# Kernel optimization log

Measured on AMD Instinct MI355X. Metric: run time of the kernel, lower is better.

The kernel has to match this reference:

```python
import jax, jax.numpy as jnp
import numpy as np

N_NODES = 100000
N_EDGES = 1600000
IN_DIM = 64
HID_DIM = 32


def setup_inputs() -> dict:
    key = jax.random.key(0)
    k1, k2, k3, k4 = jax.random.split(key, 4)
    features = jax.random.normal(k1, (N_NODES, IN_DIM), dtype=jnp.float32)
    src = jax.random.randint(k2, (N_EDGES,), 0, N_NODES, dtype=jnp.int32)
    dst = jax.random.randint(k3, (N_EDGES,), 0, N_NODES, dtype=jnp.int32)
    # Glorot-uniform weight as in DGL GraphConv reset_parameters
    limit = (6.0 / (IN_DIM + HID_DIM)) ** 0.5
    W = jax.random.uniform(k4, (IN_DIM, HID_DIM), dtype=jnp.float32,
                           minval=-limit, maxval=limit)
    b = jnp.zeros((HID_DIM,), dtype=jnp.float32)
    return {"features": features, "src": src, "dst": dst, "W": W, "b": b}


def reference(features, src, dst, W, b):
    """DGL GraphConv(norm='both', activation=relu):
    out = relu(D_in^{-1/2} A D_out^{-1/2} (X W) + b)
    (weight applied first since in_dim > out_dim)."""
    n = features.shape[0]
    ones = jnp.ones(src.shape[0], dtype=features.dtype)
    deg_out = jax.ops.segment_sum(ones, src, num_segments=n)  # out-degree
    deg_in = jax.ops.segment_sum(ones, dst, num_segments=n)   # in-degree
    norm_src = jnp.clip(deg_out, 1.0, None) ** -0.5          # [N]
    norm_dst = jnp.clip(deg_in, 1.0, None) ** -0.5           # [N]

    h = (features @ W) * norm_src[:, None]                    # [N, hid]
    msg = h[src]                                              # [E, hid] gather
    agg = jax.ops.segment_sum(msg, dst, num_segments=n)       # [N, hid] scatter-add
    out = agg * norm_dst[:, None] + b
    return jax.nn.relu(out)
```

## Files before the change

kernel.cpp:

```cpp
#include <hip/hip_runtime.h>
#include <hip/hip_fp16.h>

#define IN_DIM 64
#define HID 32
#define SHIFT 8
#define BKEYS 256
#define CAP 4608
#define HCAP 2560
#define CHUNK 8192
#define MAXB 512

__global__ __launch_bounds__(512) void multisplit_kernel(
    const int* __restrict__ src, const int* __restrict__ dst, int E, int NB,
    unsigned* __restrict__ gcur_d, unsigned* __restrict__ gcur_s,
    unsigned* __restrict__ bkt_pairs, unsigned* __restrict__ bkt_srcs)
{
    __shared__ unsigned hist_d[MAXB], cur_d[MAXB], gb_d[MAXB];
    __shared__ unsigned hist_s[MAXB], cur_s[MAXB], gb_s[MAXB];
    int t = threadIdx.x;
    int e0 = blockIdx.x * CHUNK;
    int cnt = min(CHUNK, E - e0);
    hist_d[t] = 0; hist_s[t] = 0; cur_d[t] = 0; cur_s[t] = 0;
    __syncthreads();
    const int4* s4 = (const int4*)(src + e0);
    const int4* d4 = (const int4*)(dst + e0);
    int n4 = cnt >> 2;
    for (int i = t; i < n4; i += 512) {
        int4 d = d4[i]; int4 s = s4[i];
        atomicAdd(&hist_d[d.x >> SHIFT], 1u); atomicAdd(&hist_s[s.x >> SHIFT], 1u);
        atomicAdd(&hist_d[d.y >> SHIFT], 1u); atomicAdd(&hist_s[s.y >> SHIFT], 1u);
        atomicAdd(&hist_d[d.z >> SHIFT], 1u); atomicAdd(&hist_s[s.z >> SHIFT], 1u);
        atomicAdd(&hist_d[d.w >> SHIFT], 1u); atomicAdd(&hist_s[s.w >> SHIFT], 1u);
    }
    for (int i = (n4 << 2) + t; i < cnt; i += 512) {
        atomicAdd(&hist_d[dst[e0 + i] >> SHIFT], 1u);
        atomicAdd(&hist_s[src[e0 + i] >> SHIFT], 1u);
    }
    __syncthreads();
    if (t < NB) {
        unsigned hd = hist_d[t], hs = hist_s[t];
        if (hd) gb_d[t] = atomicAdd(&gcur_d[t], hd);
        if (hs) gb_s[t] = atomicAdd(&gcur_s[t], hs);
    }
    __syncthreads();
    for (int i = t; i < n4; i += 512) {
        int4 d = d4[i]; int4 s = s4[i];
        int dv[4] = {d.x, d.y, d.z, d.w};
        int sv[4] = {s.x, s.y, s.z, s.w};
#pragma unroll
        for (int j = 0; j < 4; ++j) {
            int kd = dv[j] >> SHIFT;
            unsigned pos = gb_d[kd] + atomicAdd(&cur_d[kd], 1u);
            if (pos < CAP)
                bkt_pairs[(size_t)kd * CAP + pos] =
                    (((unsigned)dv[j] & (BKEYS - 1)) << 17) | (unsigned)sv[j];
            int ks = sv[j] >> SHIFT;
            unsigned pos2 = gb_s[ks] + atomicAdd(&cur_s[ks], 1u);
            if (pos2 < CAP) bkt_srcs[(size_t)ks * CAP + pos2] = (unsigned)sv[j];
        }
    }
    for (int i = (n4 << 2) + t; i < cnt; i += 512) {
        int dv = dst[e0 + i], sv = src[e0 + i];
        int kd = dv >> SHIFT;
        unsigned pos = gb_d[kd] + atomicAdd(&cur_d[kd], 1u);
        if (pos < CAP)
            bkt_pairs[(size_t)kd * CAP + pos] =
                (((unsigned)dv & (BKEYS - 1)) << 17) | (unsigned)sv;
        int ks = sv >> SHIFT;
        unsigned pos2 = gb_s[ks] + atomicAdd(&cur_s[ks], 1u);
        if (pos2 < CAP) bkt_srcs[(size_t)ks * CAP + pos2] = (unsigned)sv;
    }
}

__global__ __launch_bounds__(256) void degxw_kernel(
    const unsigned* __restrict__ bkt_srcs, const unsigned* __restrict__ gcur_s,
    const float* __restrict__ X, const float* __restrict__ W,
    int N, unsigned short* __restrict__ h16)
{
    __shared__ float Ws[IN_DIM * HID];
    __shared__ unsigned cnt[128];
    __shared__ float nrm[128];
    int t = threadIdx.x;
    int blk = blockIdx.x, bin = blk >> 1;
    unsigned half = blk & 1;
    ((float4*)Ws)[t]       = ((const float4*)W)[t];
    ((float4*)Ws)[t + 256] = ((const float4*)W)[t + 256];
    if (t < 128) cnt[t] = 0;
    __syncthreads();
    unsigned m = gcur_s[bin];
    if (m > CAP) m = CAP;
    const unsigned* bs = bkt_srcs + (size_t)bin * CAP;
    for (unsigned i = t; i < m; i += 256) {
        unsigned k = bs[i] & (BKEYS - 1);
        if ((k >> 7) == half) atomicAdd(&cnt[k & 127], 1u);
    }
    __syncthreads();
    if (t < 128) nrm[t] = rsqrtf(fmaxf((float)cnt[t], 1.0f));
    __syncthreads();
    int q = t & 7, ln = t >> 3;
#pragma unroll
    for (int pass = 0; pass < 4; ++pass) {
        int lv = pass * 32 + ln;
        int v = bin * BKEYS + (int)half * 128 + lv;
        if (v < N) {
            const float4* Xr = (const float4*)(X + (size_t)v * IN_DIM);
            float4 acc = make_float4(0.f, 0.f, 0.f, 0.f);
#pragma unroll
            for (int kk = 0; kk < 16; ++kk) {
                float4 xv = Xr[kk];
                int k0 = kk * 4;
                float4 w0 = ((float4*)Ws)[(k0 + 0) * 8 + q];
                float4 w1 = ((float4*)Ws)[(k0 + 1) * 8 + q];
                float4 w2 = ((float4*)Ws)[(k0 + 2) * 8 + q];
                float4 w3 = ((float4*)Ws)[(k0 + 3) * 8 + q];
                acc.x += xv.x * w0.x + xv.y * w1.x + xv.z * w2.x + xv.w * w3.x;
                acc.y += xv.x * w0.y + xv.y * w1.y + xv.z * w2.y + xv.w * w3.y;
                acc.z += xv.x * w0.z + xv.y * w1.z + xv.z * w2.z + xv.w * w3.z;
                acc.w += xv.x * w0.w + xv.y * w1.w + xv.z * w2.w + xv.w * w3.w;
            }
            float s = nrm[lv];
            __half2 a  = __floats2half2_rn(acc.x * s, acc.y * s);
            __half2 b2 = __floats2half2_rn(acc.z * s, acc.w * s);
            uint2 u;
            u.x = *(unsigned*)&a;
            u.y = *(unsigned*)&b2;
            ((uint2*)h16)[(size_t)v * 8 + q] = u;
        }
    }
}

__global__ __launch_bounds__(256) void csrgather_kernel(
    const unsigned* __restrict__ bkt_pairs, const unsigned* __restrict__ gcur_d,
    const unsigned short* __restrict__ h16, const float* __restrict__ bias,
    float* __restrict__ out, int N)
{
    __shared__ unsigned cnt[128], ex[128], cur[128];
    __shared__ unsigned ecsr[HCAP];
    __shared__ float bsh[HID];
    int t = threadIdx.x;
    int blk = blockIdx.x, bin = blk >> 1;
    unsigned half = blk & 1;
    if (t < 128) { cnt[t] = 0; cur[t] = 0; }
    if (t < HID) bsh[t] = bias[t];
    __syncthreads();
    unsigned m = gcur_d[bin];
    if (m > CAP) m = CAP;
    const unsigned* bp = bkt_pairs + (size_t)bin * CAP;
    for (unsigned i = t; i < m; i += 256) {
        unsigned k = bp[i] >> 17;
        if ((k >> 7) == half) atomicAdd(&cnt[k & 127], 1u);
    }
    __syncthreads();
    if (t < 128) ex[t] = cnt[t];
    __syncthreads();
    for (int off = 1; off < 128; off <<= 1) {
        unsigned u = (t >= off && t < 128) ? ex[t - off] : 0;
        __syncthreads();
        if (t < 128) ex[t] += u;
        __syncthreads();
    }
    for (unsigned i = t; i < m; i += 256) {
        unsigned p = bp[i];
        unsigned k = p >> 17;
        if ((k >> 7) == half) {
            unsigned kk = k & 127;
            unsigned pos = (ex[kk] - cnt[kk]) + atomicAdd(&cur[kk], 1u);
            if (pos < HCAP) ecsr[pos] = p & 0x1FFFFu;
        }
    }
    __syncthreads();
    int lane = t & 63, w = t >> 6;
    int hsel = lane >> 5, slot = (lane >> 2) & 7, q = lane & 3;
    for (int j = 0; j < 16; ++j) {
        int lv = w * 32 + j * 2 + hsel;
        unsigned dg = cnt[lv];
        unsigned st = ex[lv] - dg;
        unsigned en = st + dg; if (en > HCAP) en = HCAP;
        float a0=0.f,a1=0.f,a2=0.f,a3=0.f,a4=0.f,a5=0.f,a6=0.f,a7=0.f;
        for (unsigned u = st + slot; u < en; u += 8) {
            unsigned s = ecsr[u];
            uint4 hv = ((const uint4*)h16)[(size_t)s * 4 + q];
            __half2* hp = (__half2*)&hv;
            float2 f0 = __half22float2(hp[0]);
            float2 f1 = __half22float2(hp[1]);
            float2 f2 = __half22float2(hp[2]);
            float2 f3 = __half22float2(hp[3]);
            a0 += f0.x; a1 += f0.y; a2 += f1.x; a3 += f1.y;
            a4 += f2.x; a5 += f2.y; a6 += f3.x; a7 += f3.y;
        }
#pragma unroll
        for (int off = 4; off <= 16; off <<= 1) {
            a0 += __shfl_xor(a0, off, 64); a1 += __shfl_xor(a1, off, 64);
            a2 += __shfl_xor(a2, off, 64); a3 += __shfl_xor(a3, off, 64);
            a4 += __shfl_xor(a4, off, 64); a5 += __shfl_xor(a5, off, 64);
            a6 += __shfl_xor(a6, off, 64); a7 += __shfl_xor(a7, off, 64);
        }
        int v = bin * BKEYS + (int)half * 128 + lv;
        if (slot == 0 && v < N) {
            float nv = rsqrtf(fmaxf((float)dg, 1.0f));
            const float* bq = bsh + q * 8;
            float4 o0, o1;
            o0.x = fmaxf(a0 * nv + bq[0], 0.f);
            o0.y = fmaxf(a1 * nv + bq[1], 0.f);
            o0.z = fmaxf(a2 * nv + bq[2], 0.f);
            o0.w = fmaxf(a3 * nv + bq[3], 0.f);
            o1.x = fmaxf(a4 * nv + bq[4], 0.f);
            o1.y = fmaxf(a5 * nv + bq[5], 0.f);
            o1.z = fmaxf(a6 * nv + bq[6], 0.f);
            o1.w = fmaxf(a7 * nv + bq[7], 0.f);
            float* op = out + (size_t)v * HID + q * 8;
            *(float4*)op = o0;
            *(float4*)(op + 4) = o1;
        }
    }
}

extern "C" void kernel_launch(void* const* d_in, const int* in_sizes, int n_in,
                              void* d_out, int out_size, void* d_ws, size_t ws_size,
                              hipStream_t stream) {
    const float* X   = (const float*)d_in[0];
    const int*   src = (const int*)d_in[1];
    const int*   dst = (const int*)d_in[2];
    const float* W   = (const float*)d_in[3];
    const float* b   = (const float*)d_in[4];
    float* out = (float*)d_out;

    int N = in_sizes[0] / IN_DIM;
    int E = in_sizes[1];
    int NB = (N + BKEYS - 1) / BKEYS;

    unsigned* gcur_d = (unsigned*)d_ws;
    unsigned* gcur_s = gcur_d + MAXB;
    unsigned* bkt_pairs = gcur_s + MAXB;
    unsigned* bkt_srcs  = bkt_pairs + (size_t)NB * CAP;
    unsigned short* h16 = (unsigned short*)(bkt_srcs + (size_t)NB * CAP);

    hipMemsetAsync(gcur_d, 0, 2 * MAXB * sizeof(unsigned), stream);

    multisplit_kernel<<<(E + CHUNK - 1) / CHUNK, 512, 0, stream>>>(
        src, dst, E, NB, gcur_d, gcur_s, bkt_pairs, bkt_srcs);
    degxw_kernel<<<NB * 2, 256, 0, stream>>>(bkt_srcs, gcur_s, X, W, N, h16);
    csrgather_kernel<<<NB * 2, 256, 0, stream>>>(bkt_pairs, gcur_d, h16, b, out, N);
}
```

Baseline: 164.3 us.

## Compact src buckets to bytes, widen blocks to 512, unroll gather, replace memset

The source-degree buckets now hold only the low 8 bits of each source id as a byte rather than a full 32-bit word, which cuts write and read traffic for degree counting; the counting loop reads four bytes at a time. degxw and csrgather now run with 512 threads per block, each thread covering fewer nodes, and the gather loop is unrolled by two so two independent h16 loads are in flight. The hipMemsetAsync is replaced by a small zero kernel. The wider blocks may lower occupancy, and unaligned tails are handled by scalar fallback loops.

```diff
diff --git a/kernel.cpp b/kernel.cpp
--- a/kernel.cpp
+++ b/kernel.cpp
@@ -10,10 +10,14 @@
 #define CHUNK 8192
 #define MAXB 512
 
+__global__ void zero_kernel(unsigned* __restrict__ p) {
+    p[threadIdx.x + blockIdx.x * 256] = 0u;
+}
+
 __global__ __launch_bounds__(512) void multisplit_kernel(
     const int* __restrict__ src, const int* __restrict__ dst, int E, int NB,
     unsigned* __restrict__ gcur_d, unsigned* __restrict__ gcur_s,
-    unsigned* __restrict__ bkt_pairs, unsigned* __restrict__ bkt_srcs)
+    unsigned* __restrict__ bkt_pairs, unsigned char* __restrict__ bkt_srcs)
 {
     __shared__ unsigned hist_d[MAXB], cur_d[MAXB], gb_d[MAXB];
     __shared__ unsigned hist_s[MAXB], cur_s[MAXB], gb_s[MAXB];
@@ -56,7 +60,8 @@
                     (((unsigned)dv[j] & (BKEYS - 1)) << 17) | (unsigned)sv[j];
             int ks = sv[j] >> SHIFT;
             unsigned pos2 = gb_s[ks] + atomicAdd(&cur_s[ks], 1u);
-            if (pos2 < CAP) bkt_srcs[(size_t)ks * CAP + pos2] = (unsigned)sv[j];
+            if (pos2 < CAP)
+                bkt_srcs[(size_t)ks * CAP + pos2] = (unsigned char)(sv[j] & (BKEYS - 1));
         }
     }
     for (int i = (n4 << 2) + t; i < cnt; i += 512) {
@@ -68,12 +73,13 @@
                 (((unsigned)dv & (BKEYS - 1)) << 17) | (unsigned)sv;
         int ks = sv >> SHIFT;
         unsigned pos2 = gb_s[ks] + atomicAdd(&cur_s[ks], 1u);
-        if (pos2 < CAP) bkt_srcs[(size_t)ks * CAP + pos2] = (unsigned)sv;
-    }
-}
-
-__global__ __launch_bounds__(256) void degxw_kernel(
-    const unsigned* __restrict__ bkt_srcs, const unsigned* __restrict__ gcur_s,
+        if (pos2 < CAP)
+            bkt_srcs[(size_t)ks * CAP + pos2] = (unsigned char)(sv & (BKEYS - 1));
+    }
+}
+
+__global__ __launch_bounds__(512) void degxw_kernel(
+    const unsigned char* __restrict__ bkt_srcs, const unsigned* __restrict__ gcur_s,
     const float* __restrict__ X, const float* __restrict__ W,
     int N, unsigned short* __restrict__ h16)
 {
@@ -83,15 +89,23 @@
     int t = threadIdx.x;
     int blk = blockIdx.x, bin = blk >> 1;
     unsigned half = blk & 1;
-    ((float4*)Ws)[t]       = ((const float4*)W)[t];
-    ((float4*)Ws)[t + 256] = ((const float4*)W)[t + 256];
+    ((float4*)Ws)[t] = ((const float4*)W)[t];
     if (t < 128) cnt[t] = 0;
     __syncthreads();
     unsigned m = gcur_s[bin];
     if (m > CAP) m = CAP;
-    const unsigned* bs = bkt_srcs + (size_t)bin * CAP;
-    for (unsigned i = t; i < m; i += 256) {
-        unsigned k = bs[i] & (BKEYS - 1);
+    const unsigned char* bs = bkt_srcs + (size_t)bin * CAP;
+    const uchar4* bs4 = (const uchar4*)bs;
+    unsigned m4 = m >> 2;
+    for (unsigned i = t; i < m4; i += 512) {
+        uchar4 kk = bs4[i];
+        if ((kk.x >> 7) == half) atomicAdd(&cnt[kk.x & 127], 1u);
+        if ((kk.y >> 7) == half) atomicAdd(&cnt[kk.y & 127], 1u);
+        if ((kk.z >> 7) == half) atomicAdd(&cnt[kk.z & 127], 1u);
+        if ((kk.w >> 7) == half) atomicAdd(&cnt[kk.w & 127], 1u);
+    }
+    for (unsigned i = (m4 << 2) + t; i < m; i += 512) {
+        unsigned k = bs[i];
         if ((k >> 7) == half) atomicAdd(&cnt[k & 127], 1u);
     }
     __syncthreads();
@@ -99,8 +113,8 @@
     __syncthreads();
     int q = t & 7, ln = t >> 3;
 #pragma unroll
-    for (int pass = 0; pass < 4; ++pass) {
-        int lv = pass * 32 + ln;
+    for (int pass = 0; pass < 2; ++pass) {
+        int lv = pass * 64 + ln;
         int v = bin * BKEYS + (int)half * 128 + lv;
         if (v < N) {
             const float4* Xr = (const float4*)(X + (size_t)v * IN_DIM);
@@ -129,7 +143,7 @@
     }
 }
 
-__global__ __launch_bounds__(256) void csrgather_kernel(
+__global__ __launch_bounds__(512) void csrgather_kernel(
     const unsigned* __restrict__ bkt_pairs, const unsigned* __restrict__ gcur_d,
     const unsigned short* __restrict__ h16, const float* __restrict__ bias,
     float* __restrict__ out, int N)
@@ -141,12 +155,12 @@
     int blk = blockIdx.x, bin = blk >> 1;
     unsigned half = blk & 1;
     if (t < 128) { cnt[t] = 0; cur[t] = 0; }
-    if (t < HID) bsh[t] = bias[t];
+    if (t >= 128 && t < 128 + HID) bsh[t - 128] = bias[t - 128];
     __syncthreads();
     unsigned m = gcur_d[bin];
     if (m > CAP) m = CAP;
     const unsigned* bp = bkt_pairs + (size_t)bin * CAP;
-    for (unsigned i = t; i < m; i += 256) {
+    for (unsigned i = t; i < m; i += 512) {
         unsigned k = bp[i] >> 17;
         if ((k >> 7) == half) atomicAdd(&cnt[k & 127], 1u);
     }
@@ -159,7 +173,7 @@
         if (t < 128) ex[t] += u;
         __syncthreads();
     }
-    for (unsigned i = t; i < m; i += 256) {
+    for (unsigned i = t; i < m; i += 512) {
         unsigned p = bp[i];
         unsigned k = p >> 17;
         if ((k >> 7) == half) {
@@ -171,13 +185,30 @@
     __syncthreads();
     int lane = t & 63, w = t >> 6;
     int hsel = lane >> 5, slot = (lane >> 2) & 7, q = lane & 3;
-    for (int j = 0; j < 16; ++j) {
-        int lv = w * 32 + j * 2 + hsel;
+    for (int j = 0; j < 8; ++j) {
+        int lv = w * 16 + j * 2 + hsel;
         unsigned dg = cnt[lv];
         unsigned st = ex[lv] - dg;
         unsigned en = st + dg; if (en > HCAP) en = HCAP;
         float a0=0.f,a1=0.f,a2=0.f,a3=0.f,a4=0.f,a5=0.f,a6=0.f,a7=0.f;
-        for (unsigned u = st + slot; u < en; u += 8) {
+        unsigned u = st + slot;
+        for (; u + 8 < en; u += 16) {
+            unsigned s0 = ecsr[u];
+            unsigned s1 = ecsr[u + 8];
+            uint4 hv0 = ((const uint4*)h16)[(size_t)s0 * 4 + q];
+            uint4 hv1 = ((const uint4*)h16)[(size_t)s1 * 4 + q];
+            __half2* hp0 = (__half2*)&hv0;
+            __half2* hp1 = (__half2*)&hv1;
+            float2 f0 = __half22float2(hp0[0]), g0 = __half22float2(hp1[0]);
+            float2 f1 = __half22float2(hp0[1]), g1 = __half22float2(hp1[1]);
+            float2 f2 = __half22float2(hp0[2]), g2 = __half22float2(hp1[2]);
+            float2 f3 = __half22float2(hp0[3]), g3 = __half22float2(hp1[3]);
+            a0 += f0.x + g0.x; a1 += f0.y + g0.y;
+            a2 += f1.x + g1.x; a3 += f1.y + g1.y;
+            a4 += f2.x + g2.x; a5 += f2.y + g2.y;
+            a6 += f3.x + g3.x; a7 += f3.y + g3.y;
+        }
+        if (u < en) {
             unsigned s = ecsr[u];
             uint4 hv = ((const uint4*)h16)[(size_t)s * 4 + q];
             __half2* hp = (__half2*)&hv;
@@ -232,13 +263,12 @@
     unsigned* gcur_d = (unsigned*)d_ws;
     unsigned* gcur_s = gcur_d + MAXB;
     unsigned* bkt_pairs = gcur_s + MAXB;
-    unsigned* bkt_srcs  = bkt_pairs + (size_t)NB * CAP;
+    unsigned char* bkt_srcs = (unsigned char*)(bkt_pairs + (size_t)NB * CAP);
     unsigned short* h16 = (unsigned short*)(bkt_srcs + (size_t)NB * CAP);
 
-    hipMemsetAsync(gcur_d, 0, 2 * MAXB * sizeof(unsigned), stream);
-
+    zero_kernel<<<4, 256, 0, stream>>>(gcur_d);
     multisplit_kernel<<<(E + CHUNK - 1) / CHUNK, 512, 0, stream>>>(
         src, dst, E, NB, gcur_d, gcur_s, bkt_pairs, bkt_srcs);
-    degxw_kernel<<<NB * 2, 256, 0, stream>>>(bkt_srcs, gcur_s, X, W, N, h16);
-    csrgather_kernel<<<NB * 2, 256, 0, stream>>>(bkt_pairs, gcur_d, h16, b, out, N);
-}
+    degxw_kernel<<<NB * 2, 512, 0, stream>>>(bkt_srcs, gcur_s, X, W, N, h16);
+    csrgather_kernel<<<NB * 2, 512, 0, stream>>>(bkt_pairs, gcur_d, h16, b, out, N);
+}
```

New measurement: 149.6 us. 1.1x faster.
